# Performance work log

Hardware: AMD Instinct MI355X
Metric: run time of the kernel (lower is better)

The kernel has to match this reference:

```python
import jax, jax.numpy as jnp
import numpy as np

B, N, F, U, E = 4, 10000, 128, 128, 160000


def setup_inputs() -> dict:
    key = jax.random.key(0)
    ks = jax.random.split(key, 5)
    s = lambda d: 1.0 / np.sqrt(d)
    return {
        "node_features": jax.random.normal(ks[0], (B, N, F), dtype=jnp.float32),
        "edge_indices": jax.random.randint(ks[1], (E, 2), 0, N, dtype=jnp.int64),
        "W_t": jax.random.normal(ks[2], (F, U), dtype=jnp.float32) * s(F),
        "b_t": jnp.zeros((U,), jnp.float32),
        "W_a": jax.random.normal(ks[3], (2 * U, 1), dtype=jnp.float32) * s(2 * U),
        "b_a": jnp.zeros((1,), jnp.float32),
        "W_c": jax.random.normal(ks[4], (2 * U, U), dtype=jnp.float32) * s(2 * U),
        "b_c": jnp.zeros((U,), jnp.float32),
    }


def reference(node_features, edge_indices, W_t, b_t, W_a, b_a, W_c, b_c):
    b, n, _ = node_features.shape
    e = edge_indices.shape[0]
    u = W_t.shape[1]
    # transform: Dense + relu  [B,N,U]
    h = jax.nn.relu(jnp.einsum('bnf,fu->bnu', node_features, W_t) + b_t)
    src = edge_indices[:, 0]
    tgt = edge_indices[:, 1]
    source_nodes = h[:, src, :]   # [B,E,U]
    target_nodes = h[:, tgt, :]   # [B,E,U]
    edge_features = jnp.concatenate([source_nodes, target_nodes], axis=-1)  # [B,E,2U]
    att = jnp.tanh(jnp.einsum('beu,uo->beo', edge_features, W_a) + b_a)     # [B,E,1]
    # original softmax is over axis=0 of the flattened [B*E,1] tensor
    attn = jax.nn.softmax(att.reshape(-1, 1), axis=0).reshape(b, e, 1)
    weighted = attn * target_nodes  # [B,E,U]
    # scatter-add messages onto source nodes, per batch element
    scattered = jax.vmap(lambda m: jax.ops.segment_sum(m, src, num_segments=n))(weighted)  # [B,N,U]
    out = jax.nn.relu(
        jnp.einsum('bnu,uo->bno', jnp.concatenate([h, scattered], axis=-1), W_c) + b_c
    )
    return out
```

## Files before the change

### kernel.cpp

```cpp
#include <hip/hip_runtime.h>

#define BB 4
#define NN 10000
#define FF 128
#define UU 128
#define EE 160000

typedef __bf16 bf16x8 __attribute__((ext_vector_type(8)));
typedef float  f32x4  __attribute__((ext_vector_type(4)));

#define WS_S      0
#define WS_DEG    256
#define WS_OFFS   40448
#define WS_CUR    80640
#define WS_TGT    120832
#define WS_EXW    760832
#define WS_P      3320832
#define WS_Q      3480832
#define WS_BTG    3640832
#define WS_BCG    3673600
#define WS_HS     3739136

__global__ __launch_bounds__(256) void k_prep(const float* __restrict__ Wt,
                                              const float* __restrict__ Wc,
                                              char* __restrict__ ws) {
  const int gid = blockIdx.x * 256 + threadIdx.x;
  uint4* zp = (uint4*)ws;
  uint4 z = {0u, 0u, 0u, 0u};
  for (int i = gid; i < 2528; i += 2048) zp[i] = z;

  __bf16* Btg = (__bf16*)(ws + WS_BTG);
  __bf16* Bcg = (__bf16*)(ws + WS_BCG);
  {
    int i = gid;
    int n = i & 127, kb8 = i >> 7;
    int kc = kb8 >> 2, kbq = kb8 & 3;
    int lane = (n & 15) | (kbq << 4), c = n >> 4;
    const float* src = Wt + (size_t)kb8 * 8 * 128 + n;
    bf16x8 v;
#pragma unroll
    for (int j = 0; j < 8; ++j) v[j] = (__bf16)src[(size_t)j * 128];
    *(bf16x8*)(Btg + ((kc * 8 + c) * 512 + lane * 8)) = v;
  }
#pragma unroll
  for (int it = 0; it < 2; ++it) {
    int i = gid + it * 2048;
    int n = i & 127, kb8 = i >> 7;
    int kc = kb8 >> 2, kbq = kb8 & 3;
    int lane = (n & 15) | (kbq << 4), c = n >> 4;
    const float* src = Wc + (size_t)kb8 * 8 * 128 + n;
    bf16x8 v;
#pragma unroll
    for (int j = 0; j < 8; ++j) v[j] = (__bf16)src[(size_t)j * 128];
    *(bf16x8*)(Bcg + ((kc * 8 + c) * 512 + lane * 8)) = v;
  }
}

__global__ __launch_bounds__(256) void k_gemm_h(
    const float* __restrict__ nf, const __bf16* __restrict__ Btg,
    const float* __restrict__ bt, const float* __restrict__ Wa,
    const int* __restrict__ eidx, int* __restrict__ deg,
    __bf16* __restrict__ hs, float* __restrict__ p2, float* __restrict__ q2) {
  {
    int e = blockIdx.x * 256 + threadIdx.x;
    atomicAdd(&deg[eidx[2 * e]], 1);
  }
  __shared__ __bf16 Bt[32 * 512];
  const int tid = threadIdx.x;
  {
    uint4* d = (uint4*)Bt;
    const uint4* s = (const uint4*)Btg;
#pragma unroll
    for (int i = tid; i < 2048; i += 256) d[i] = s[i];
  }
  __syncthreads();

  const int wid = tid >> 6, lane = tid & 63;
  const int lr = lane & 15, lg = lane >> 4;
  const int row0 = blockIdx.x * 64 + wid * 16;

  f32x4 acc[8];
#pragma unroll
  for (int c = 0; c < 8; ++c)
#pragma unroll
    for (int r = 0; r < 4; ++r) acc[c][r] = 0.f;

#pragma unroll
  for (int k0 = 0; k0 < 128; k0 += 32) {
    int kk = k0 + lg * 8;
    const float4* ap = (const float4*)(nf + (size_t)(row0 + lr) * 128 + kk);
    float4 a0 = ap[0], a1 = ap[1];
    bf16x8 af;
    af[0] = (__bf16)a0.x; af[1] = (__bf16)a0.y; af[2] = (__bf16)a0.z; af[3] = (__bf16)a0.w;
    af[4] = (__bf16)a1.x; af[5] = (__bf16)a1.y; af[6] = (__bf16)a1.z; af[7] = (__bf16)a1.w;
#pragma unroll
    for (int c = 0; c < 8; ++c) {
      bf16x8 bf = *(const bf16x8*)(Bt + (((k0 >> 5) << 3) + c) * 512 + lane * 8);
      acc[c] = __builtin_amdgcn_mfma_f32_16x16x32_bf16(af, bf, acc[c], 0, 0, 0);
    }
  }

#pragma unroll
  for (int r = 0; r < 4; ++r) {
    int row = row0 + lg * 4 + r;
    int b = row / NN;
    int n = row - b * NN;
    size_t dst = ((size_t)n * 4 + b) * 256;
    float pr = 0.f, qr = 0.f;
#pragma unroll
    for (int c = 0; c < 8; ++c) {
      int col = c * 16 + lr;
      float v = acc[c][r] + bt[col];
      v = fmaxf(v, 0.f);
      hs[dst + col] = (__bf16)v;
      pr += v * Wa[col];
      qr += v * Wa[128 + col];
    }
#pragma unroll
    for (int m = 1; m < 16; m <<= 1) {
      pr += __shfl_xor(pr, m);
      qr += __shfl_xor(qr, m);
    }
    if (lr == 0) {
      p2[n * 4 + b] = pr;
      q2[n * 4 + b] = qr;
    }
  }
}

__global__ __launch_bounds__(1024) void k_scan(const int* __restrict__ deg,
                                               int* __restrict__ offs,
                                               int* __restrict__ cursor) {
  const int t = threadIdx.x, lane = t & 63, wv = t >> 6;
  const int base = t * 10;
  int local[10];
  int s = 0;
#pragma unroll
  for (int i = 0; i < 10; ++i) {
    int v = (base + i < NN) ? deg[base + i] : 0;
    local[i] = s;
    s += v;
  }
  const int tsum = s;
#pragma unroll
  for (int off = 1; off < 64; off <<= 1) {
    int v = __shfl_up(s, off);
    if (lane >= off) s += v;
  }
  __shared__ int wsum[16];
  if (lane == 63) wsum[wv] = s;
  __syncthreads();
  int add = 0;
#pragma unroll
  for (int w = 0; w < 16; ++w) {
    int v = wsum[w];
    if (w < wv) add += v;
  }
  int pre = add + s - tsum;
#pragma unroll
  for (int i = 0; i < 10; ++i) {
    int idx = base + i;
    if (idx < NN) {
      int o = pre + local[i];
      offs[idx] = o;
      cursor[idx] = o;
    }
  }
  if (t == 1023) offs[NN] = pre + tsum;
}

__global__ __launch_bounds__(256) void k_att(const int* __restrict__ eidx,
                                             const float4* __restrict__ p2,
                                             const float4* __restrict__ q2,
                                             const float* __restrict__ ba,
                                             int* __restrict__ cursor,
                                             int* __restrict__ tgts,
                                             float4* __restrict__ exw,
                                             float* __restrict__ S) {
  int e = blockIdx.x * 256 + threadIdx.x;
  int s = eidx[2 * e], t = eidx[2 * e + 1];
  float4 pv = p2[s];
  float4 qv = q2[t];
  float bias = ba[0];
#define ATT(pc, qc, out)                              \
  {                                                   \
    float a = (pc) + (qc) + bias;                     \
    float z = __expf(2.f * a);                        \
    float th = 1.f - __fdividef(2.f, z + 1.f);        \
    (out) = __expf(th);                               \
  }
  float v0, v1, v2, v3;
  ATT(pv.x, qv.x, v0)
  ATT(pv.y, qv.y, v1)
  ATT(pv.z, qv.z, v2)
  ATT(pv.w, qv.w, v3)
#undef ATT
  int pos = atomicAdd(&cursor[s], 1);
  tgts[pos] = t;
  exw[pos] = make_float4(v0, v1, v2, v3);
  float vs = v0 + v1 + v2 + v3;
#pragma unroll
  for (int m = 1; m < 64; m <<= 1) vs += __shfl_xor(vs, m);
  __shared__ float part[4];
  int wid = threadIdx.x >> 6, lane = threadIdx.x & 63;
  if (lane == 0) part[wid] = vs;
  __syncthreads();
  if (threadIdx.x == 0) atomicAdd(S, part[0] + part[1] + part[2] + part[3]);
}

__global__ __launch_bounds__(256) void k_agg(
    const int* __restrict__ tgts, const int* __restrict__ offs,
    const float4* __restrict__ exw, const float* __restrict__ S,
    __bf16* __restrict__ hs) {
  const int wid = threadIdx.x >> 6, lane = threadIdx.x & 63;
  const int n = blockIdx.x * 4 + wid;
  const int myb = lane >> 4, sub = lane & 15;
  const int o0 = offs[n], o1 = offs[n + 1];
  const uint4* __restrict__ hu4 = (const uint4*)hs;
  float acc[8];
#pragma unroll
  for (int i = 0; i < 8; ++i) acc[i] = 0.f;

  const int lbase = myb * 32 + sub;
  for (int base = o0; base < o1; base += 64) {
    int il = base + lane;
    int t_l = 0;
    float4 wv = {0.f, 0.f, 0.f, 0.f};
    if (il < o1) {
      t_l = tgts[il];
      wv = exw[il];
    }
    int cnt = min(64, o1 - base);
    for (int j = 0; j < cnt; j += 2) {
      int t0 = __shfl(t_l, j), t1 = __shfl(t_l, j + 1);
      float w0x = __shfl(wv.x, j), w0y = __shfl(wv.y, j);
      float w0z = __shfl(wv.z, j), w0w = __shfl(wv.w, j);
      float w1x = __shfl(wv.x, j + 1), w1y = __shfl(wv.y, j + 1);
      float w1z = __shfl(wv.z, j + 1), w1w = __shfl(wv.w, j + 1);
      uint4 va = hu4[(size_t)t0 * 128 + lbase];
      uint4 vb = hu4[(size_t)t1 * 128 + lbase];
      float mw0 = (myb == 0) ? w0x : (myb == 1) ? w0y : (myb == 2) ? w0z : w0w;
      float mw1 = (myb == 0) ? w1x : (myb == 1) ? w1y : (myb == 2) ? w1z : w1w;
#define LO(x) __uint_as_float((x) << 16)
#define HI(x) __uint_as_float((x)&0xffff0000u)
      acc[0] = fmaf(mw0, LO(va.x), acc[0]); acc[1] = fmaf(mw0, HI(va.x), acc[1]);
      acc[2] = fmaf(mw0, LO(va.y), acc[2]); acc[3] = fmaf(mw0, HI(va.y), acc[3]);
      acc[4] = fmaf(mw0, LO(va.z), acc[4]); acc[5] = fmaf(mw0, HI(va.z), acc[5]);
      acc[6] = fmaf(mw0, LO(va.w), acc[6]); acc[7] = fmaf(mw0, HI(va.w), acc[7]);
      acc[0] = fmaf(mw1, LO(vb.x), acc[0]); acc[1] = fmaf(mw1, HI(vb.x), acc[1]);
      acc[2] = fmaf(mw1, LO(vb.y), acc[2]); acc[3] = fmaf(mw1, HI(vb.y), acc[3]);
      acc[4] = fmaf(mw1, LO(vb.z), acc[4]); acc[5] = fmaf(mw1, HI(vb.z), acc[5]);
      acc[6] = fmaf(mw1, LO(vb.w), acc[6]); acc[7] = fmaf(mw1, HI(vb.w), acc[7]);
#undef LO
#undef HI
    }
  }
  const float invS = 1.0f / S[0];
  uint4 st;
  unsigned* sp = (unsigned*)&st;
#pragma unroll
  for (int i = 0; i < 4; ++i) {
    unsigned ux = __float_as_uint(acc[2 * i] * invS);
    ux = (ux + 0x7fffu + ((ux >> 16) & 1u)) >> 16;
    unsigned uy = __float_as_uint(acc[2 * i + 1] * invS);
    uy = (uy + 0x7fffu + ((uy >> 16) & 1u)) >> 16;
    sp[i] = ux | (uy << 16);
  }
  ((uint4*)hs)[(size_t)n * 128 + myb * 32 + 16 + sub] = st;
}

__global__ __launch_bounds__(256) void k_gemm_out(
    const __bf16* __restrict__ hs, const __bf16* __restrict__ Bcg,
    const float* __restrict__ bc, float* __restrict__ out) {
  __shared__ __bf16 Bt[64 * 512];
  const int tid = threadIdx.x;
  {
    uint4* d = (uint4*)Bt;
    const uint4* s = (const uint4*)Bcg;
#pragma unroll
    for (int i = tid; i < 4096; i += 256) d[i] = s[i];
  }
  __syncthreads();

  const int wid = tid >> 6, lane = tid & 63;
  const int lr = lane & 15, lg = lane >> 4;
  const int row0 = blockIdx.x * 128 + wid * 32;

  f32x4 acc[2][8];
#pragma unroll
  for (int t = 0; t < 2; ++t)
#pragma unroll
    for (int c = 0; c < 8; ++c)
#pragma unroll
      for (int r = 0; r < 4; ++r) acc[t][c][r] = 0.f;

  int ra = min(row0 + lr, 39999);
  int rb = min(row0 + 16 + lr, 39999);

#pragma unroll
  for (int k0 = 0; k0 < 256; k0 += 32) {
    int kk = k0 + lg * 8;
    bf16x8 af0 = *(const bf16x8*)(hs + (size_t)ra * 256 + kk);
    bf16x8 af1 = *(const bf16x8*)(hs + (size_t)rb * 256 + kk);
#pragma unroll
    for (int c = 0; c < 8; ++c) {
      bf16x8 bf = *(const bf16x8*)(Bt + (((k0 >> 5) << 3) + c) * 512 + lane * 8);
      acc[0][c] = __builtin_amdgcn_mfma_f32_16x16x32_bf16(af0, bf, acc[0][c], 0, 0, 0);
      acc[1][c] = __builtin_amdgcn_mfma_f32_16x16x32_bf16(af1, bf, acc[1][c], 0, 0, 0);
    }
  }

#pragma unroll
  for (int t = 0; t < 2; ++t)
#pragma unroll
    for (int r = 0; r < 4; ++r) {
      int m = row0 + t * 16 + lg * 4 + r;
      if (m < 40000) {
        int n = m >> 2, b = m & 3;
        size_t orow = ((size_t)b * NN + n) * 128;
#pragma unroll
        for (int c = 0; c < 8; ++c) {
          int col = c * 16 + lr;
          float v = acc[t][c][r] + bc[col];
          out[orow + col] = fmaxf(v, 0.f);
        }
      }
    }
}

extern "C" void kernel_launch(void* const* d_in, const int* in_sizes, int n_in,
                              void* d_out, int out_size, void* d_ws,
                              size_t ws_size, hipStream_t stream) {
  const float* nf = (const float*)d_in[0];
  const int* eidx = (const int*)d_in[1];
  const float* Wt = (const float*)d_in[2];
  const float* bt = (const float*)d_in[3];
  const float* Wa = (const float*)d_in[4];
  const float* ba = (const float*)d_in[5];
  const float* Wc = (const float*)d_in[6];
  const float* bc = (const float*)d_in[7];
  float* out = (float*)d_out;

  char* w = (char*)d_ws;
  float* S = (float*)(w + WS_S);
  int* deg = (int*)(w + WS_DEG);
  int* offs = (int*)(w + WS_OFFS);
  int* cursor = (int*)(w + WS_CUR);
  int* tgts = (int*)(w + WS_TGT);
  float4* exw = (float4*)(w + WS_EXW);
  float* p2 = (float*)(w + WS_P);
  float* q2 = (float*)(w + WS_Q);
  __bf16* Btg = (__bf16*)(w + WS_BTG);
  __bf16* Bcg = (__bf16*)(w + WS_BCG);
  __bf16* hs = (__bf16*)(w + WS_HS);

  k_prep<<<8, 256, 0, stream>>>(Wt, Wc, w);
  k_gemm_h<<<625, 256, 0, stream>>>(nf, Btg, bt, Wa, eidx, deg, hs, p2, q2);
  k_scan<<<1, 1024, 0, stream>>>(deg, offs, cursor);
  k_att<<<625, 256, 0, stream>>>(eidx, (const float4*)p2, (const float4*)q2,
                                 ba, cursor, tgts, exw, S);
  k_agg<<<2500, 256, 0, stream>>>(tgts, offs, exw, S, hs);
  k_gemm_out<<<313, 256, 0, stream>>>(hs, Bcg, bc, out);
}
```

Before: 164.5 us.

## Transpose edge weights to planar layout and unroll aggregation four edges per step

Edge attention weights are now stored in four per-batch planes instead of float4 records. The aggregation kernel loads 16 edges per chunk, with each lane fetching only its own batch's weight, and processes four gathers per iteration to raise memory-level parallelism. Both GEMM kernels move to 512-thread blocks with one 16-row tile per wave, which needs bounds guards and clamping. The planar layout makes the scattered stores in the attention kernel four separate writes, and the GEMM change lowers per-wave register use at the cost of fewer rows of work per wave.

```diff
diff --git a/kernel.cpp b/kernel.cpp
--- a/kernel.cpp
+++ b/kernel.cpp
@@ -56,14 +56,14 @@
   }
 }
 
-__global__ __launch_bounds__(256) void k_gemm_h(
+__global__ __launch_bounds__(512) void k_gemm_h(
     const float* __restrict__ nf, const __bf16* __restrict__ Btg,
     const float* __restrict__ bt, const float* __restrict__ Wa,
     const int* __restrict__ eidx, int* __restrict__ deg,
     __bf16* __restrict__ hs, float* __restrict__ p2, float* __restrict__ q2) {
   {
-    int e = blockIdx.x * 256 + threadIdx.x;
-    atomicAdd(&deg[eidx[2 * e]], 1);
+    int e = blockIdx.x * 512 + threadIdx.x;
+    if (e < EE) atomicAdd(&deg[eidx[2 * e]], 1);
   }
   __shared__ __bf16 Bt[32 * 512];
   const int tid = threadIdx.x;
@@ -71,24 +71,26 @@
     uint4* d = (uint4*)Bt;
     const uint4* s = (const uint4*)Btg;
 #pragma unroll
-    for (int i = tid; i < 2048; i += 256) d[i] = s[i];
+    for (int i = tid; i < 2048; i += 512) d[i] = s[i];
   }
   __syncthreads();
 
   const int wid = tid >> 6, lane = tid & 63;
   const int lr = lane & 15, lg = lane >> 4;
-  const int row0 = blockIdx.x * 64 + wid * 16;
+  const int row0 = blockIdx.x * 128 + wid * 16;
 
   f32x4 acc[8];
 #pragma unroll
   for (int c = 0; c < 8; ++c)
 #pragma unroll
     for (int r = 0; r < 4; ++r) acc[c][r] = 0.f;
+
+  const int arow = min(row0 + lr, 39999);
 
 #pragma unroll
   for (int k0 = 0; k0 < 128; k0 += 32) {
     int kk = k0 + lg * 8;
-    const float4* ap = (const float4*)(nf + (size_t)(row0 + lr) * 128 + kk);
+    const float4* ap = (const float4*)(nf + (size_t)arow * 128 + kk);
     float4 a0 = ap[0], a1 = ap[1];
     bf16x8 af;
     af[0] = (__bf16)a0.x; af[1] = (__bf16)a0.y; af[2] = (__bf16)a0.z; af[3] = (__bf16)a0.w;
@@ -103,6 +105,7 @@
 #pragma unroll
   for (int r = 0; r < 4; ++r) {
     int row = row0 + lg * 4 + r;
+    bool ok = row < 40000;
     int b = row / NN;
     int n = row - b * NN;
     size_t dst = ((size_t)n * 4 + b) * 256;
@@ -112,7 +115,7 @@
       int col = c * 16 + lr;
       float v = acc[c][r] + bt[col];
       v = fmaxf(v, 0.f);
-      hs[dst + col] = (__bf16)v;
+      if (ok) hs[dst + col] = (__bf16)v;
       pr += v * Wa[col];
       qr += v * Wa[128 + col];
     }
@@ -121,7 +124,7 @@
       pr += __shfl_xor(pr, m);
       qr += __shfl_xor(qr, m);
     }
-    if (lr == 0) {
+    if (lr == 0 && ok) {
       p2[n * 4 + b] = pr;
       q2[n * 4 + b] = qr;
     }
@@ -175,7 +178,7 @@
                                              const float* __restrict__ ba,
                                              int* __restrict__ cursor,
                                              int* __restrict__ tgts,
-                                             float4* __restrict__ exw,
+                                             float* __restrict__ exwT,
                                              float* __restrict__ S) {
   int e = blockIdx.x * 256 + threadIdx.x;
   int s = eidx[2 * e], t = eidx[2 * e + 1];
@@ -197,7 +200,10 @@
 #undef ATT
   int pos = atomicAdd(&cursor[s], 1);
   tgts[pos] = t;
-  exw[pos] = make_float4(v0, v1, v2, v3);
+  exwT[pos] = v0;
+  exwT[EE + pos] = v1;
+  exwT[2 * EE + pos] = v2;
+  exwT[3 * EE + pos] = v3;
   float vs = v0 + v1 + v2 + v3;
 #pragma unroll
   for (int m = 1; m < 64; m <<= 1) vs += __shfl_xor(vs, m);
@@ -210,7 +216,7 @@
 
 __global__ __launch_bounds__(256) void k_agg(
     const int* __restrict__ tgts, const int* __restrict__ offs,
-    const float4* __restrict__ exw, const float* __restrict__ S,
+    const float* __restrict__ exwT, const float* __restrict__ S,
     __bf16* __restrict__ hs) {
   const int wid = threadIdx.x >> 6, lane = threadIdx.x & 63;
   const int n = blockIdx.x * 4 + wid;
@@ -222,35 +228,42 @@
   for (int i = 0; i < 8; ++i) acc[i] = 0.f;
 
   const int lbase = myb * 32 + sub;
-  for (int base = o0; base < o1; base += 64) {
-    int il = base + lane;
-    int t_l = 0;
-    float4 wv = {0.f, 0.f, 0.f, 0.f};
-    if (il < o1) {
-      t_l = tgts[il];
-      wv = exw[il];
-    }
-    int cnt = min(64, o1 - base);
-    for (int j = 0; j < cnt; j += 2) {
-      int t0 = __shfl(t_l, j), t1 = __shfl(t_l, j + 1);
-      float w0x = __shfl(wv.x, j), w0y = __shfl(wv.y, j);
-      float w0z = __shfl(wv.z, j), w0w = __shfl(wv.w, j);
-      float w1x = __shfl(wv.x, j + 1), w1y = __shfl(wv.y, j + 1);
-      float w1z = __shfl(wv.z, j + 1), w1w = __shfl(wv.w, j + 1);
+  const int wsrc = myb << 4;
+  for (int base = o0; base < o1; base += 16) {
+    int idx = base + sub;
+    bool valid = idx < o1;
+    int t_l = valid ? tgts[idx] : 0;
+    float w_l = valid ? exwT[(size_t)myb * EE + idx] : 0.f;
+    int cnt = min(16, o1 - base);
+    for (int j = 0; j < cnt; j += 4) {
+      int t0 = __shfl(t_l, j + 0);
+      int t1 = __shfl(t_l, j + 1);
+      int t2 = __shfl(t_l, j + 2);
+      int t3 = __shfl(t_l, j + 3);
+      float m0 = __shfl(w_l, wsrc | (j + 0));
+      float m1 = __shfl(w_l, wsrc | (j + 1));
+      float m2 = __shfl(w_l, wsrc | (j + 2));
+      float m3 = __shfl(w_l, wsrc | (j + 3));
       uint4 va = hu4[(size_t)t0 * 128 + lbase];
       uint4 vb = hu4[(size_t)t1 * 128 + lbase];
-      float mw0 = (myb == 0) ? w0x : (myb == 1) ? w0y : (myb == 2) ? w0z : w0w;
-      float mw1 = (myb == 0) ? w1x : (myb == 1) ? w1y : (myb == 2) ? w1z : w1w;
+      uint4 vc = hu4[(size_t)t2 * 128 + lbase];
+      uint4 vd = hu4[(size_t)t3 * 128 + lbase];
 #define LO(x) __uint_as_float((x) << 16)
 #define HI(x) __uint_as_float((x)&0xffff0000u)
-      acc[0] = fmaf(mw0, LO(va.x), acc[0]); acc[1] = fmaf(mw0, HI(va.x), acc[1]);
-      acc[2] = fmaf(mw0, LO(va.y), acc[2]); acc[3] = fmaf(mw0, HI(va.y), acc[3]);
-      acc[4] = fmaf(mw0, LO(va.z), acc[4]); acc[5] = fmaf(mw0, HI(va.z), acc[5]);
-      acc[6] = fmaf(mw0, LO(va.w), acc[6]); acc[7] = fmaf(mw0, HI(va.w), acc[7]);
-      acc[0] = fmaf(mw1, LO(vb.x), acc[0]); acc[1] = fmaf(mw1, HI(vb.x), acc[1]);
-      acc[2] = fmaf(mw1, LO(vb.y), acc[2]); acc[3] = fmaf(mw1, HI(vb.y), acc[3]);
-      acc[4] = fmaf(mw1, LO(vb.z), acc[4]); acc[5] = fmaf(mw1, HI(vb.z), acc[5]);
-      acc[6] = fmaf(mw1, LO(vb.w), acc[6]); acc[7] = fmaf(mw1, HI(vb.w), acc[7]);
+#define ACC(m, v)                                                   \
+  acc[0] = fmaf((m), LO((v).x), acc[0]);                            \
+  acc[1] = fmaf((m), HI((v).x), acc[1]);                            \
+  acc[2] = fmaf((m), LO((v).y), acc[2]);                            \
+  acc[3] = fmaf((m), HI((v).y), acc[3]);                            \
+  acc[4] = fmaf((m), LO((v).z), acc[4]);                            \
+  acc[5] = fmaf((m), HI((v).z), acc[5]);                            \
+  acc[6] = fmaf((m), LO((v).w), acc[6]);                            \
+  acc[7] = fmaf((m), HI((v).w), acc[7]);
+      ACC(m0, va)
+      ACC(m1, vb)
+      ACC(m2, vc)
+      ACC(m3, vd)
+#undef ACC
 #undef LO
 #undef HI
     }
@@ -269,7 +282,7 @@
   ((uint4*)hs)[(size_t)n * 128 + myb * 32 + 16 + sub] = st;
 }
 
-__global__ __launch_bounds__(256) void k_gemm_out(
+__global__ __launch_bounds__(512) void k_gemm_out(
     const __bf16* __restrict__ hs, const __bf16* __restrict__ Bcg,
     const float* __restrict__ bc, float* __restrict__ out) {
   __shared__ __bf16 Bt[64 * 512];
@@ -278,54 +291,47 @@
     uint4* d = (uint4*)Bt;
     const uint4* s = (const uint4*)Bcg;
 #pragma unroll
-    for (int i = tid; i < 4096; i += 256) d[i] = s[i];
+    for (int i = tid; i < 4096; i += 512) d[i] = s[i];
   }
   __syncthreads();
 
   const int wid = tid >> 6, lane = tid & 63;
   const int lr = lane & 15, lg = lane >> 4;
-  const int row0 = blockIdx.x * 128 + wid * 32;
-
-  f32x4 acc[2][8];
-#pragma unroll
-  for (int t = 0; t < 2; ++t)
-#pragma unroll
-    for (int c = 0; c < 8; ++c)
-#pragma unroll
-      for (int r = 0; r < 4; ++r) acc[t][c][r] = 0.f;
-
-  int ra = min(row0 + lr, 39999);
-  int rb = min(row0 + 16 + lr, 39999);
+  const int row0 = blockIdx.x * 128 + wid * 16;
+
+  f32x4 acc[8];
+#pragma unroll
+  for (int c = 0; c < 8; ++c)
+#pragma unroll
+    for (int r = 0; r < 4; ++r) acc[c][r] = 0.f;
+
+  const int arow = min(row0 + lr, 39999);
 
 #pragma unroll
   for (int k0 = 0; k0 < 256; k0 += 32) {
     int kk = k0 + lg * 8;
-    bf16x8 af0 = *(const bf16x8*)(hs + (size_t)ra * 256 + kk);
-    bf16x8 af1 = *(const bf16x8*)(hs + (size_t)rb * 256 + kk);
+    bf16x8 af = *(const bf16x8*)(hs + (size_t)arow * 256 + kk);
 #pragma unroll
     for (int c = 0; c < 8; ++c) {
       bf16x8 bf = *(const bf16x8*)(Bt + (((k0 >> 5) << 3) + c) * 512 + lane * 8);
-      acc[0][c] = __builtin_amdgcn_mfma_f32_16x16x32_bf16(af0, bf, acc[0][c], 0, 0, 0);
-      acc[1][c] = __builtin_amdgcn_mfma_f32_16x16x32_bf16(af1, bf, acc[1][c], 0, 0, 0);
-    }
-  }
-
-#pragma unroll
-  for (int t = 0; t < 2; ++t)
-#pragma unroll
-    for (int r = 0; r < 4; ++r) {
-      int m = row0 + t * 16 + lg * 4 + r;
-      if (m < 40000) {
-        int n = m >> 2, b = m & 3;
-        size_t orow = ((size_t)b * NN + n) * 128;
-#pragma unroll
-        for (int c = 0; c < 8; ++c) {
-          int col = c * 16 + lr;
-          float v = acc[t][c][r] + bc[col];
-          out[orow + col] = fmaxf(v, 0.f);
-        }
+      acc[c] = __builtin_amdgcn_mfma_f32_16x16x32_bf16(af, bf, acc[c], 0, 0, 0);
+    }
+  }
+
+#pragma unroll
+  for (int r = 0; r < 4; ++r) {
+    int m = row0 + lg * 4 + r;
+    if (m < 40000) {
+      int n = m >> 2, b = m & 3;
+      size_t orow = ((size_t)b * NN + n) * 128;
+#pragma unroll
+      for (int c = 0; c < 8; ++c) {
+        int col = c * 16 + lr;
+        float v = acc[c][r] + bc[col];
+        out[orow + col] = fmaxf(v, 0.f);
       }
     }
+  }
 }
 
 extern "C" void kernel_launch(void* const* d_in, const int* in_sizes, int n_in,
@@ -347,7 +353,7 @@
   int* offs = (int*)(w + WS_OFFS);
   int* cursor = (int*)(w + WS_CUR);
   int* tgts = (int*)(w + WS_TGT);
-  float4* exw = (float4*)(w + WS_EXW);
+  float* exwT = (float*)(w + WS_EXW);
   float* p2 = (float*)(w + WS_P);
   float* q2 = (float*)(w + WS_Q);
   __bf16* Btg = (__bf16*)(w + WS_BTG);
@@ -355,10 +361,10 @@
   __bf16* hs = (__bf16*)(w + WS_HS);
 
   k_prep<<<8, 256, 0, stream>>>(Wt, Wc, w);
-  k_gemm_h<<<625, 256, 0, stream>>>(nf, Btg, bt, Wa, eidx, deg, hs, p2, q2);
+  k_gemm_h<<<313, 512, 0, stream>>>(nf, Btg, bt, Wa, eidx, deg, hs, p2, q2);
   k_scan<<<1, 1024, 0, stream>>>(deg, offs, cursor);
   k_att<<<625, 256, 0, stream>>>(eidx, (const float4*)p2, (const float4*)q2,
-                                 ba, cursor, tgts, exw, S);
-  k_agg<<<2500, 256, 0, stream>>>(tgts, offs, exw, S, hs);
-  k_gemm_out<<<313, 256, 0, stream>>>(hs, Bcg, bc, out);
-}
+                                 ba, cursor, tgts, exwT, S);
+  k_agg<<<2500, 256, 0, stream>>>(tgts, offs, exwT, S, hs);
+  k_gemm_out<<<313, 512, 0, stream>>>(hs, Bcg, bc, out);
+}
```

Measured after the change: 160.7 us. -2.3%, faster.
